# Optimization experiments

Measured on AMD Instinct MI355X. Metric: run time of the kernel, lower is better.

Reference implementation:

```python
import jax, jax.numpy as jnp
import numpy as np

THRESH = 0.5
DECAY = 0.25
LENS = 0.5

@jax.custom_vjp
def spike(x):
    return (x > THRESH).astype(x.dtype)

def _spike_fwd(x):
    return (x > THRESH).astype(x.dtype), x

def _spike_bwd(x, g):
    return (g * (jnp.abs(x - THRESH) < LENS).astype(g.dtype),)

spike.defvjp(_spike_fwd, _spike_bwd)

def mem_update(x):
    # LIF neuron over leading time dim: x [T, ...] -> binary spikes [T, ...]
    def step(carry, xt):
        mem_prev, s_prev = carry
        mem = mem_prev * DECAY * (1.0 - jax.lax.stop_gradient(s_prev)) + xt
        s = spike(mem)
        return (mem, s), s
    init = (jnp.zeros_like(x[0]), jnp.zeros_like(x[0]))
    _, out = jax.lax.scan(step, init, x)
    return out

def conv_bn(x, w, s, b):
    # 1x1 conv (bias=False) + frozen BN folded into per-channel scale/shift
    # x: [TB, C_in, H, W], w: [C_out, C_in]
    y = jnp.einsum('bchw,oc->bohw', x, w)
    return y * s[None, :, None, None] + b[None, :, None, None]

NUM_HEADS = 8

def setup_inputs() -> dict:
    key = jax.random.key(0)
    ks = jax.random.split(key, 16)
    T, B, C, H, W = 4, 8, 512, 24, 24
    Cv = 4 * C
    N = H * W
    inp = {}
    inp['x'] = jax.random.normal(ks[0], (T, B, C, H, W), jnp.float32)
    inp['s_pos_embed'] = 0.02 * jax.random.normal(ks[1], (1, C, N), jnp.float32)
    inp['q_w'] = jax.random.normal(ks[2], (C, C), jnp.float32) / np.sqrt(C)
    inp['q_s'] = 1.0 + 0.1 * jax.random.normal(ks[3], (C,), jnp.float32)
    inp['q_b'] = 0.1 * jax.random.normal(ks[4], (C,), jnp.float32)
    inp['k_w'] = jax.random.normal(ks[5], (C, C), jnp.float32) / np.sqrt(C)
    inp['k_s'] = 1.0 + 0.1 * jax.random.normal(ks[6], (C,), jnp.float32)
    inp['k_b'] = 0.1 * jax.random.normal(ks[7], (C,), jnp.float32)
    inp['v_w'] = jax.random.normal(ks[8], (Cv, C), jnp.float32) / np.sqrt(C)
    inp['v_s'] = 1.0 + 0.1 * jax.random.normal(ks[9], (Cv,), jnp.float32)
    inp['v_b'] = 0.1 * jax.random.normal(ks[10], (Cv,), jnp.float32)
    inp['p_w'] = jax.random.normal(ks[11], (C, Cv), jnp.float32) / np.sqrt(Cv)
    inp['p_s'] = 1.0 + 0.1 * jax.random.normal(ks[12], (C,), jnp.float32)
    inp['p_b'] = 0.1 * jax.random.normal(ks[13], (C,), jnp.float32)
    return inp

def reference(x, s_pos_embed, q_w, q_s, q_b, k_w, k_s, k_b, v_w, v_s, v_b, p_w, p_s, p_b):
    T, B, C, H, W = x.shape
    N = H * W
    Cv = v_w.shape[0]
    dh = C // NUM_HEADS
    scale = dh ** -0.5

    # positional encoding ('search' branch) + head spike
    x = x.reshape(T, B, C, N) + s_pos_embed
    x = mem_update(x).reshape(T * B, C, H, W)

    q = conv_bn(x, q_w, q_s, q_b).reshape(T, B, C, N)
    k = conv_bn(x, k_w, k_s, k_b).reshape(T, B, C, N)
    v = conv_bn(x, v_w, v_s, v_b).reshape(T, B, Cv, N)

    def to_heads(t, nc):
        # [T,B,c,N] -> [T,B,heads,N,c//heads]
        return t.transpose(0, 1, 3, 2).reshape(T, B, N, NUM_HEADS, nc // NUM_HEADS).transpose(0, 1, 3, 2, 4)

    q = to_heads(mem_update(q), C)
    k = to_heads(mem_update(k), C)
    v = to_heads(mem_update(v), Cv)

    # linear attention: (k^T @ v) then q @ (.)
    kv = jnp.einsum('tbhnd,tbhne->tbhde', k, v)
    o = jnp.einsum('tbhnd,tbhde->tbhne', q, kv) * (scale * 2.0)

    o = o.transpose(0, 1, 3, 2, 4).reshape(T, B, N, Cv).transpose(0, 1, 3, 2).reshape(T, B, Cv, H, W)
    o = mem_update(o)
    out = conv_bn(o.reshape(T * B, Cv, H, W), p_w, p_s, p_b).reshape(T, B, C, H, W)
    return out
```

## Files before the change

kernel.cpp:

```cpp
#include <hip/hip_runtime.h>
#include <cstdint>

#define T_DIM 4
#define B_DIM 8
#define C_DIM 512
#define N_DIM 576
#define CV_DIM 2048
#define TB_DIM 32
#define NW 9

typedef unsigned long long u64;
typedef unsigned char u8;
typedef uint32_t u32;
typedef _Float16 h16;
typedef __attribute__((ext_vector_type(8))) _Float16 f16x8;
typedef __attribute__((ext_vector_type(16))) float f32x16;

__device__ __forceinline__ void gload16(const void* gp, void* lp) {
    __builtin_amdgcn_global_load_lds(
        (const __attribute__((address_space(1))) void*)gp,
        (__attribute__((address_space(3))) void*)lp, 16, 0, 0);
}

__global__ __launch_bounds__(256) void lif_x_T(const float* __restrict__ x,
                                               const float* __restrict__ pos,
                                               h16* __restrict__ sxT) {
    const int ct = blockIdx.x, nt = blockIdx.y, b = blockIdx.z;
    const int c0 = ct * 64, n0 = nt * 64;
    __shared__ h16 T[64][64];
    const int tid = threadIdx.x;
    const int n_l = tid & 63, cg = tid >> 6;
    const int row = tid >> 2, q = tid & 3;

    float pv[16], mem[16], spk[16];
    #pragma unroll
    for (int ii = 0; ii < 16; ++ii) {
        pv[ii] = pos[(c0 + cg * 16 + ii) * N_DIM + n0 + n_l];
        mem[ii] = 0.f; spk[ii] = 0.f;
    }
    for (int t = 0; t < T_DIM; ++t) {
        #pragma unroll
        for (int ii = 0; ii < 16; ++ii) {
            float xt = x[((size_t)(t * B_DIM + b) * C_DIM + c0 + cg * 16 + ii) * N_DIM + n0 + n_l] + pv[ii];
            mem[ii] = mem[ii] * 0.25f * (1.f - spk[ii]) + xt;
            spk[ii] = (mem[ii] > 0.5f) ? 1.f : 0.f;
            T[n_l][cg * 16 + ii] = (h16)spk[ii];
        }
        __syncthreads();
        {
            h16* dst = sxT + ((size_t)(t * B_DIM + b) * N_DIM + n0 + row) * C_DIM + c0;
            const int f = row & 7;
            #pragma unroll
            for (int e = 0; e < 2; ++e) {
                int gl = q + e * 4;
                uint4 v = *(const uint4*)&T[row][gl * 8];
                *(uint4*)(dst + (gl ^ f) * 8) = v;
            }
        }
        __syncthreads();
    }
}

__global__ __launch_bounds__(256) void split_qkv(const float* __restrict__ q_w,
                                                 const float* __restrict__ k_w,
                                                 const float* __restrict__ v_w,
                                                 h16* __restrict__ wp) {
    int i = blockIdx.x * 256 + threadIdx.x;
    int row = i >> 6;
    int g = i & 63;
    int g8 = g * 8;
    const float* src = (row < 512) ? q_w + (size_t)row * 512
                     : (row < 1024) ? k_w + (size_t)(row - 512) * 512
                                    : v_w + (size_t)(row - 1024) * 512;
    float4 a = *(const float4*)(src + g8);
    float4 bq = *(const float4*)(src + g8 + 4);
    float v[8] = {a.x, a.y, a.z, a.w, bq.x, bq.y, bq.z, bq.w};
    f16x8 vh, vl;
    #pragma unroll
    for (int j = 0; j < 8; ++j) {
        float w = v[j] * 4096.f;
        h16 h1 = (h16)w;
        vh[j] = h1;
        vl[j] = (h16)(w - (float)h1);
    }
    int permcol = (g & ~7) * 8 + ((g & 7) ^ (row & 7)) * 8;
    *(f16x8*)(wp + (size_t)row * 512 + permcol) = vh;
    *(f16x8*)(wp + (size_t)3072 * 512 + (size_t)row * 512 + permcol) = vl;
}

__global__ __launch_bounds__(256) void split_p(const float* __restrict__ p_w,
                                               h16* __restrict__ wp) {
    int i = blockIdx.x * 256 + threadIdx.x;
    int row = i >> 8;
    int g = i & 255;
    int g8 = g * 8;
    const float* src = p_w + (size_t)row * 2048;
    float4 a = *(const float4*)(src + g8);
    float4 bq = *(const float4*)(src + g8 + 4);
    float v[8] = {a.x, a.y, a.z, a.w, bq.x, bq.y, bq.z, bq.w};
    f16x8 vh;
    #pragma unroll
    for (int j = 0; j < 8; ++j)
        vh[j] = (h16)(v[j] * 4096.f);
    int permcol = (g & ~7) * 8 + ((g & 7) ^ (row & 7)) * 8;
    *(f16x8*)(wp + (size_t)row * 2048 + permcol) = vh;
}

__global__ __launch_bounds__(256) void concat_sb(const float* __restrict__ qs, const float* __restrict__ qb,
                                                 const float* __restrict__ ks, const float* __restrict__ kb,
                                                 const float* __restrict__ vs, const float* __restrict__ vb,
                                                 float* __restrict__ sc, float* __restrict__ bi) {
    int i = blockIdx.x * 256 + threadIdx.x;
    if (i >= 3072) return;
    if (i < 512)       { sc[i] = qs[i];        bi[i] = qb[i]; }
    else if (i < 1024) { sc[i] = ks[i - 512];  bi[i] = kb[i - 512]; }
    else               { sc[i] = vs[i - 1024]; bi[i] = vb[i - 1024]; }
}

__global__ __launch_bounds__(256, 3) void gemm_qkv_mfma(
        const h16* __restrict__ wp,
        const h16* __restrict__ sxT,
        const float* __restrict__ sc,
        const float* __restrict__ bi,
        u32* __restrict__ qkvb32)
{
    __shared__ h16 Ah[2][128][64];
    __shared__ h16 Bh[T_DIM][32][64];

    const int lin = blockIdx.x + 24 * (blockIdx.y + 18 * blockIdx.z);
    const int xcd = lin & 7, idx = lin >> 3;
    const int m0  = (3 * xcd + idx % 3) * 128;
    const int r2  = idx / 3;
    const int b   = r2 / 18;
    const int wq2 = r2 % 18;

    const int tid = threadIdx.x;
    const int lane = tid & 63;
    const int wv   = tid >> 6;
    const int l31  = lane & 31;
    const int lhi  = lane >> 5;

    const h16* aB = wp + ((size_t)(m0 + (tid >> 3))) * 512 + (tid & 7) * 8;
    const h16* bB = sxT + ((size_t)b * N_DIM + wq2 * 32 + (tid >> 3)) * 512 + (tid & 7) * 8;
    char* ldsA = (char*)&Ah[0][0][0];
    char* ldsB = (char*)&Bh[0][0][0];
    const int woff = wv * 1024;

    f32x16 acc[T_DIM];
    #pragma unroll
    for (int t = 0; t < T_DIM; ++t) acc[t] = (f32x16)(0.f);

    for (int k0 = 0; k0 < 512; k0 += 64) {
        #pragma unroll
        for (int i = 0; i < 8; ++i)
            gload16(aB + ((size_t)(i >> 2) * 3072 + (i & 3) * 32) * 512 + k0,
                    ldsA + i * 4096 + woff);
        #pragma unroll
        for (int i = 0; i < 4; ++i)
            gload16(bB + (size_t)i * (B_DIM * N_DIM) * 512 + k0,
                    ldsB + i * 4096 + woff);
        __syncthreads();

        const int fsw = l31 & 7;
        #pragma unroll
        for (int s = 0; s < 4; ++s) {
            const int g = ((s * 2 + lhi) ^ fsw) * 8;
            f16x8 a0 = *(const f16x8*)&Ah[0][wv * 32 + l31][g];
            f16x8 a1 = *(const f16x8*)&Ah[1][wv * 32 + l31][g];
            #pragma unroll
            for (int t = 0; t < T_DIM; ++t) {
                f16x8 bt = *(const f16x8*)&Bh[t][l31][g];
                acc[t] = __builtin_amdgcn_mfma_f32_32x32x16_f16(a0, bt, acc[t], 0, 0, 0);
                acc[t] = __builtin_amdgcn_mfma_f32_32x32x16_f16(a1, bt, acc[t], 0, 0, 0);
            }
        }
        __syncthreads();
    }

    const float inv = 0x1p-12f;
    #pragma unroll
    for (int r = 0; r < 16; ++r) {
        int row = m0 + wv * 32 + (r & 3) + 8 * (r >> 2) + 4 * lhi;
        float scv = sc[row], biv = bi[row];
        float mem = 0.f, spk = 0.f;
        #pragma unroll
        for (int t = 0; t < T_DIM; ++t) {
            float y = __fadd_rn(__fmul_rn(acc[t][r] * inv, scv), biv);
            mem = mem * 0.25f * (1.f - spk) + y;
            spk = (mem > 0.5f) ? 1.f : 0.f;
            u64 Bal = __ballot(spk > 0.f);
            u32 wrd = lhi ? (u32)(Bal >> 32) : (u32)Bal;
            if (l31 == 0)
                qkvb32[((size_t)(t * B_DIM + b) * 3072 + row) * 18 + wq2] = wrd;
        }
    }
}

__global__ __launch_bounds__(256) void kv_pop_kernel(const u64* __restrict__ bits,
                                                     h16* __restrict__ kvt) {
    int tbh = blockIdx.x;
    int tb = tbh >> 3, h = tbh & 7;
    int e = threadIdx.x;
    __shared__ u64 kb[64][NW];
    const u64* kbase = bits + ((size_t)tb * 3072 + 512 + h * 64) * NW;
    const u64* vbase = bits + ((size_t)tb * 3072 + 1024 + h * 256) * NW;
    for (int i = threadIdx.x; i < 576; i += 256) kb[i / 9][i % 9] = kbase[i];
    __syncthreads();
    u64 vr[NW];
    #pragma unroll
    for (int w = 0; w < NW; ++w) vr[w] = vbase[(size_t)e * NW + w];
    h16* outp = kvt + (size_t)tbh * 16384 + (size_t)e * 64;
    for (int d0 = 0; d0 < 64; d0 += 4) {
        ushort4 pk;
        unsigned short* pp = (unsigned short*)&pk;
        #pragma unroll
        for (int j = 0; j < 4; ++j) {
            int scnt = 0;
            #pragma unroll
            for (int w = 0; w < NW; ++w) scnt += __popcll(kb[d0 + j][w] & vr[w]);
            union { h16 h; unsigned short u; } cv;
            cv.h = (h16)scnt;
            pp[j] = cv.u;
        }
        *(ushort4*)(outp + d0) = pk;
    }
}

__global__ __launch_bounds__(256, 2) void o_attn_mfma(const u64* __restrict__ qkvb,
                                                      const h16* __restrict__ kvt,
                                                      h16* __restrict__ soT) {
    const int nw = blockIdx.x;
    const int ec = blockIdx.y;
    const int bh = blockIdx.z;
    const int b = bh >> 3, h = bh & 7;
    const int tid = threadIdx.x;
    const int lane = tid & 63, wv = tid >> 6, l31 = lane & 31, lhi = lane >> 5;

    __shared__ h16 kvs[128][64];
    __shared__ __align__(16) u64 qbs[64];
    __shared__ h16 Tr[64][136];

    const int st_row = tid >> 1;
    const int st_half = tid & 1;

    float mem0[16], spk0[16], mem1[16], spk1[16];
    #pragma unroll
    for (int r = 0; r < 16; ++r) { mem0[r] = 0.f; spk0[r] = 0.f; mem1[r] = 0.f; spk1[r] = 0.f; }

    for (int t = 0; t < T_DIM; ++t) {
        const int tb = t * B_DIM + b;
        __syncthreads();
        {
            const uint4* src = (const uint4*)(kvt + ((size_t)(tb * 8 + h) * 16384)
                                + (size_t)(ec * 128 + st_row) * 64 + st_half * 32);
            uint4 g0 = src[0], g1 = src[1], g2 = src[2], g3 = src[3];
            const int sw = st_row & 7;
            *(uint4*)&kvs[st_row][8 * ((st_half * 4 + 0) ^ sw)] = g0;
            *(uint4*)&kvs[st_row][8 * ((st_half * 4 + 1) ^ sw)] = g1;
            *(uint4*)&kvs[st_row][8 * ((st_half * 4 + 2) ^ sw)] = g2;
            *(uint4*)&kvs[st_row][8 * ((st_half * 4 + 3) ^ sw)] = g3;
        }
        if (tid < 64)
            qbs[tid] = qkvb[((size_t)tb * 3072 + h * 64 + tid) * NW + nw];
        __syncthreads();

        f32x16 acc0 = (f32x16)(0.f), acc1 = (f32x16)(0.f);
        const int er = wv * 32 + l31;
        const int esw = er & 7;
        const u32* qw32 = (const u32*)qbs;
        #pragma unroll
        for (int sub = 0; sub < 4; ++sub) {
            const int g = sub * 2 + lhi;
            f16x8 af = *(const f16x8*)&kvs[er][8 * (g ^ esw)];
            union { f16x8 v; unsigned short u[8]; } b0, b1;
            #pragma unroll
            for (int j = 0; j < 8; ++j) {
                const int d = sub * 16 + lhi * 8 + j;
                u32 w0 = qw32[d * 2 + 0];
                u32 w1 = qw32[d * 2 + 1];
                b0.u[j] = ((w0 >> l31) & 1u) ? (unsigned short)0x3C00 : (unsigned short)0;
                b1.u[j] = ((w1 >> l31) & 1u) ? (unsigned short)0x3C00 : (unsigned short)0;
            }
            acc0 = __builtin_amdgcn_mfma_f32_32x32x16_f16(af, b0.v, acc0, 0, 0, 0);
            acc1 = __builtin_amdgcn_mfma_f32_32x32x16_f16(af, b1.v, acc1, 0, 0, 0);
        }

        #pragma unroll
        for (int r = 0; r < 16; ++r) {
            mem0[r] = mem0[r] * 0.25f * (1.f - spk0[r]) + acc0[r] * 0.25f;
            spk0[r] = (mem0[r] > 0.5f) ? 1.f : 0.f;
            mem1[r] = mem1[r] * 0.25f * (1.f - spk1[r]) + acc1[r] * 0.25f;
            spk1[r] = (mem1[r] > 0.5f) ? 1.f : 0.f;
        }
        #pragma unroll
        for (int q = 0; q < 4; ++q) {
            ushort4 w0, w1;
            unsigned short* p0 = (unsigned short*)&w0;
            unsigned short* p1 = (unsigned short*)&w1;
            #pragma unroll
            for (int j = 0; j < 4; ++j) {
                union { h16 hh; unsigned short uu; } c0, c1;
                c0.hh = (h16)spk0[q * 4 + j];
                c1.hh = (h16)spk1[q * 4 + j];
                p0[j] = c0.uu;
                p1[j] = c1.uu;
            }
            int e = wv * 32 + 4 * lhi + 8 * q;
            *(ushort4*)&Tr[l31][e] = w0;
            *(ushort4*)&Tr[32 + l31][e] = w1;
        }
        __syncthreads();
        const size_t obase = ((size_t)tb * N_DIM + nw * 64) * CV_DIM + h * 256 + ec * 128;
        #pragma unroll
        for (int it = 0; it < 4; ++it) {
            int ch = it * 256 + tid;
            int n = ch >> 4, ge = ch & 15;
            uint4 v = *(const uint4*)&Tr[n][ge * 8];
            int gsw = (ge & 8) | ((ge & 7) ^ (n & 7));
            *(uint4*)(soT + obase + (size_t)n * CV_DIM + gsw * 8) = v;
        }
    }
}

__global__ __launch_bounds__(256, 3) void gemm_p_mfma(
        const h16* __restrict__ wp,
        const h16* __restrict__ soT,
        const float* __restrict__ ps,
        const float* __restrict__ pb,
        float* __restrict__ out)
{
    __shared__ h16 Ah[128][64];
    __shared__ h16 Bh[4][32][64];

    const int tbq = blockIdx.z;
    const int m0  = blockIdx.x * 128;
    const int wq2 = blockIdx.y;
    const int tid = threadIdx.x;
    const int lane = tid & 63;
    const int wv   = tid >> 6;
    const int l31  = lane & 31;
    const int lhi  = lane >> 5;

    const h16* aB = wp + ((size_t)(m0 + (tid >> 3))) * 2048 + (tid & 7) * 8;
    const h16* bB = soT + ((size_t)(tbq * 4) * N_DIM + wq2 * 32 + (tid >> 3)) * 2048 + (tid & 7) * 8;
    char* ldsA = (char*)&Ah[0][0];
    char* ldsB = (char*)&Bh[0][0][0];
    const int woff = wv * 1024;

    f32x16 acc[4];
    #pragma unroll
    for (int tt = 0; tt < 4; ++tt) acc[tt] = (f32x16)(0.f);

    for (int k0 = 0; k0 < CV_DIM; k0 += 64) {
        #pragma unroll
        for (int i = 0; i < 4; ++i)
            gload16(aB + (size_t)(i * 32) * 2048 + k0,
                    ldsA + i * 4096 + woff);
        #pragma unroll
        for (int tt = 0; tt < 4; ++tt)
            gload16(bB + (size_t)tt * (N_DIM * CV_DIM) + k0,
                    ldsB + tt * 4096 + woff);
        __syncthreads();

        const int fsw = l31 & 7;
        #pragma unroll
        for (int s = 0; s < 4; ++s) {
            const int g = ((s * 2 + lhi) ^ fsw) * 8;
            f16x8 a0 = *(const f16x8*)&Ah[wv * 32 + l31][g];
            #pragma unroll
            for (int tt = 0; tt < 4; ++tt) {
                f16x8 bt = *(const f16x8*)&Bh[tt][l31][g];
                acc[tt] = __builtin_amdgcn_mfma_f32_32x32x16_f16(a0, bt, acc[tt], 0, 0, 0);
            }
        }
        __syncthreads();
    }

    const float inv = 0x1p-12f;
    #pragma unroll
    for (int r = 0; r < 16; ++r) {
        int row = m0 + wv * 32 + (r & 3) + 8 * (r >> 2) + 4 * lhi;
        float scv = ps[row], biv = pb[row];
        #pragma unroll
        for (int tt = 0; tt < 4; ++tt) {
            float y = __fadd_rn(__fmul_rn(acc[tt][r] * inv, scv), biv);
            out[(size_t)(tbq * 4 + tt) * (C_DIM * N_DIM) + (size_t)row * N_DIM + wq2 * 32 + l31] = y;
        }
    }
}

extern "C" void kernel_launch(void* const* d_in, const int* in_sizes, int n_in,
                              void* d_out, int out_size, void* d_ws, size_t ws_size,
                              hipStream_t stream) {
    const float* x    = (const float*)d_in[0];
    const float* pos  = (const float*)d_in[1];
    const float* q_w  = (const float*)d_in[2];
    const float* q_s  = (const float*)d_in[3];
    const float* q_b  = (const float*)d_in[4];
    const float* k_w  = (const float*)d_in[5];
    const float* k_s  = (const float*)d_in[6];
    const float* k_b  = (const float*)d_in[7];
    const float* v_w  = (const float*)d_in[8];
    const float* v_s  = (const float*)d_in[9];
    const float* v_b  = (const float*)d_in[10];
    const float* p_w  = (const float*)d_in[11];
    const float* p_s  = (const float*)d_in[12];
    const float* p_b  = (const float*)d_in[13];
    float* out = (float*)d_out;

    char* ws = (char*)d_ws;
    size_t off = 0;
    u64* qkvb = (u64*)(ws + off); off += 7077888;
    h16* kvt  = (h16*)(ws + off); off += 8388608;
    h16* pw2  = (h16*)(ws + off); off += (size_t)2 * 512 * 2048 * 2;
    float* scc = (float*)(ws + off); off += 3072 * 4;
    float* bic = (float*)(ws + off); off += 3072 * 4;
    char* region = ws + off;
    h16* sxT  = (h16*)region;
    h16* qkvw = (h16*)(region + (size_t)T_DIM * B_DIM * N_DIM * C_DIM * 2);
    h16* soT  = (h16*)region;
    off += (size_t)TB_DIM * N_DIM * CV_DIM * 2;

    split_qkv<<<768, 256, 0, stream>>>(q_w, k_w, v_w, qkvw);
    split_p<<<512, 256, 0, stream>>>(p_w, pw2);
    concat_sb<<<12, 256, 0, stream>>>(q_s, q_b, k_s, k_b, v_s, v_b, scc, bic);

    dim3 gl(C_DIM / 64, N_DIM / 64, B_DIM);
    lif_x_T<<<gl, 256, 0, stream>>>(x, pos, sxT);

    dim3 gq(3072 / 128, 18, B_DIM);
    gemm_qkv_mfma<<<gq, 256, 0, stream>>>(qkvw, sxT, scc, bic, (u32*)qkvb);

    kv_pop_kernel<<<TB_DIM * 8, 256, 0, stream>>>(qkvb, kvt);
    dim3 go(NW, 2, B_DIM * 8);
    o_attn_mfma<<<go, 256, 0, stream>>>(qkvb, kvt, soT);

    dim3 gp(C_DIM / 128, 18, TB_DIM / 4);
    gemm_p_mfma<<<gp, 256, 0, stream>>>(pw2, soT, p_s, p_b, out);
}
```

Before: 244.4 us.

## Double-buffer QKV GEMM LDS tiles with K=32 steps and async prefetch

New measurement: 257.3 us. +5.3%, slower.

```diff
diff --git a/kernel.cpp b/kernel.cpp
--- a/kernel.cpp
+++ b/kernel.cpp
@@ -49,12 +49,13 @@
         __syncthreads();
         {
             h16* dst = sxT + ((size_t)(t * B_DIM + b) * N_DIM + n0 + row) * C_DIM + c0;
-            const int f = row & 7;
+            const int f = row & 3;
             #pragma unroll
             for (int e = 0; e < 2; ++e) {
                 int gl = q + e * 4;
                 uint4 v = *(const uint4*)&T[row][gl * 8];
-                *(uint4*)(dst + (gl ^ f) * 8) = v;
+                int slot = (gl & ~3) | ((gl & 3) ^ f);
+                *(uint4*)(dst + slot * 8) = v;
             }
         }
         __syncthreads();
@@ -83,7 +84,7 @@
         vh[j] = h1;
         vl[j] = (h16)(w - (float)h1);
     }
-    int permcol = (g & ~7) * 8 + ((g & 7) ^ (row & 7)) * 8;
+    int permcol = ((g & ~3) + ((g & 3) ^ (row & 3))) * 8;
     *(f16x8*)(wp + (size_t)row * 512 + permcol) = vh;
     *(f16x8*)(wp + (size_t)3072 * 512 + (size_t)row * 512 + permcol) = vl;
 }
@@ -124,8 +125,8 @@
         const float* __restrict__ bi,
         u32* __restrict__ qkvb32)
 {
-    __shared__ h16 Ah[2][128][64];
-    __shared__ h16 Bh[T_DIM][32][64];
+    __shared__ h16 Ah[2][2][128][32];
+    __shared__ h16 Bh[2][T_DIM][32][32];
 
     const int lin = blockIdx.x + 24 * (blockIdx.y + 18 * blockIdx.z);
     const int xcd = lin & 7, idx = lin >> 3;
@@ -140,42 +141,74 @@
     const int l31  = lane & 31;
     const int lhi  = lane >> 5;
 
-    const h16* aB = wp + ((size_t)(m0 + (tid >> 3))) * 512 + (tid & 7) * 8;
-    const h16* bB = sxT + ((size_t)b * N_DIM + wq2 * 32 + (tid >> 3)) * 512 + (tid & 7) * 8;
-    char* ldsA = (char*)&Ah[0][0][0];
-    char* ldsB = (char*)&Bh[0][0][0];
-    const int woff = wv * 1024;
+    const size_t APL = (size_t)3072 * 512;
+    const size_t BPL = (size_t)B_DIM * N_DIM * 512;
+
+    const h16* aS[4];
+    #pragma unroll
+    for (int i = 0; i < 4; ++i) {
+        int G = i * 256 + tid;
+        int pl = G >> 9, row = (G >> 2) & 127, gs = G & 3;
+        aS[i] = wp + (size_t)pl * APL + (size_t)(m0 + row) * 512 + gs * 8;
+    }
+    const h16* bS[2];
+    #pragma unroll
+    for (int i = 0; i < 2; ++i) {
+        int G = i * 256 + tid;
+        int tt = G >> 7, row = (G >> 2) & 31, gs = G & 3;
+        bS[i] = sxT + (size_t)tt * BPL + ((size_t)b * N_DIM + wq2 * 32 + row) * 512 + gs * 8;
+    }
 
     f32x16 acc[T_DIM];
     #pragma unroll
     for (int t = 0; t < T_DIM; ++t) acc[t] = (f32x16)(0.f);
 
-    for (int k0 = 0; k0 < 512; k0 += 64) {
-        #pragma unroll
-        for (int i = 0; i < 8; ++i)
-            gload16(aB + ((size_t)(i >> 2) * 3072 + (i & 3) * 32) * 512 + k0,
-                    ldsA + i * 4096 + woff);
-        #pragma unroll
-        for (int i = 0; i < 4; ++i)
-            gload16(bB + (size_t)i * (B_DIM * N_DIM) * 512 + k0,
-                    ldsB + i * 4096 + woff);
-        __syncthreads();
-
-        const int fsw = l31 & 7;
-        #pragma unroll
-        for (int s = 0; s < 4; ++s) {
+    {
+        char* aD = (char*)&Ah[0][0][0][0] + wv * 1024;
+        char* bD = (char*)&Bh[0][0][0][0] + wv * 1024;
+        gload16(aS[0], aD);
+        gload16(aS[1], aD + 4096);
+        gload16(aS[2], aD + 8192);
+        gload16(aS[3], aD + 12288);
+        gload16(bS[0], bD);
+        gload16(bS[1], bD + 4096);
+    }
+
+    const int fsw = l31 & 3;
+    for (int j = 0; j < 16; ++j) {
+        const int cur = j & 1;
+        __builtin_amdgcn_s_barrier();
+        if (j < 15) {
+            const int k0 = (j + 1) * 32;
+            char* aD = (char*)&Ah[cur ^ 1][0][0][0] + wv * 1024;
+            char* bD = (char*)&Bh[cur ^ 1][0][0][0] + wv * 1024;
+            gload16(aS[0] + k0, aD);
+            gload16(aS[1] + k0, aD + 4096);
+            gload16(aS[2] + k0, aD + 8192);
+            gload16(aS[3] + k0, aD + 12288);
+            gload16(bS[0] + k0, bD);
+            gload16(bS[1] + k0, bD + 4096);
+            asm volatile("s_waitcnt vmcnt(6)" ::: "memory");
+        } else {
+            asm volatile("s_waitcnt vmcnt(0)" ::: "memory");
+        }
+        __builtin_amdgcn_s_barrier();
+        __builtin_amdgcn_sched_barrier(0);
+
+        #pragma unroll
+        for (int s = 0; s < 2; ++s) {
             const int g = ((s * 2 + lhi) ^ fsw) * 8;
-            f16x8 a0 = *(const f16x8*)&Ah[0][wv * 32 + l31][g];
-            f16x8 a1 = *(const f16x8*)&Ah[1][wv * 32 + l31][g];
+            f16x8 a0 = *(const f16x8*)&Ah[cur][0][wv * 32 + l31][g];
+            f16x8 a1 = *(const f16x8*)&Ah[cur][1][wv * 32 + l31][g];
             #pragma unroll
             for (int t = 0; t < T_DIM; ++t) {
-                f16x8 bt = *(const f16x8*)&Bh[t][l31][g];
+                f16x8 bt = *(const f16x8*)&Bh[cur][t][l31][g];
                 acc[t] = __builtin_amdgcn_mfma_f32_32x32x16_f16(a0, bt, acc[t], 0, 0, 0);
                 acc[t] = __builtin_amdgcn_mfma_f32_32x32x16_f16(a1, bt, acc[t], 0, 0, 0);
             }
         }
-        __syncthreads();
-    }
+    }
+    __builtin_amdgcn_s_barrier();
 
     const float inv = 0x1p-12f;
     #pragma unroll
```
